# Optimization experiments

Measured on AMD Instinct MI355X. Metric: run time of the kernel, lower is better.

Reference implementation:

```python
import jax, jax.numpy as jnp
import numpy as np

N = 4096        # number of cells (graph nodes)
D = 128         # feature / embedding dim (isize)
NEIGHBOR = 15   # kNN column used for the distance cutoff
GAMMA = 8.0
OMEGA = 0.5


def setup_inputs() -> dict:
    key = jax.random.key(0)
    k = jax.random.split(key, 6)
    features = jax.random.normal(k[0], (N, D), dtype=jnp.float32)
    # sparse binary adjacency (~16 neighbors/node on average), stored dense
    adj = (jax.random.uniform(k[1], (N, N)) < 0.004).astype(jnp.float32)
    # symmetric positive pairwise distances
    d = jax.random.uniform(k[2], (N, N), minval=0.05, maxval=1.0)
    dis = ((d + d.T) * 0.5).astype(jnp.float32)
    scale = 1.0 / np.sqrt(D)
    W0 = (jax.random.normal(k[3], (D, D), dtype=jnp.float32) * scale)
    b0 = jnp.zeros((D,), jnp.float32)
    W1 = (jax.random.normal(k[4], (D, D), dtype=jnp.float32) * scale)
    b1 = jnp.zeros((D,), jnp.float32)
    return {"features": features, "adj": adj, "dis": dis,
            "W0": W0, "b0": b0, "W1": W1, "b1": b1}


def _gcn_layer(h, A, W, b):
    # torch_geometric GCNConv: sym-normalize (A + I), then X' = A_norm @ X @ W + b
    A_hat = A + jnp.eye(A.shape[0], dtype=A.dtype)
    deg = A_hat.sum(axis=1)
    dinv = jnp.where(deg > 0, 1.0 / jnp.sqrt(deg), 0.0)
    A_norm = dinv[:, None] * A_hat * dinv[None, :]
    return A_norm @ (h @ W) + b


def reference(features, adj, dis, W0, b0, W1, b1):
    eps = 1e-8
    # --- buffers precomputed in __init__ of the torch module ---
    d_sorted = jnp.sort(dis, axis=1)
    d_cut = jnp.median(d_sorted[:, NEIGHBOR])
    adj_mask = (dis > 0) & (dis <= d_cut)
    d_scaled = jnp.where(adj_mask, dis, jnp.inf) / d_cut
    s_d = jnp.exp(-GAMMA * d_scaled * d_scaled)   # 1/exp(g*d^2); exp(-inf)=0
    # --- internal_forward: 2 GCN layers on adj.T, relu between ---
    A = adj.T
    h = jax.nn.relu(_gcn_layer(features, A, W0, b0))
    h = _gcn_layer(h, A, W1, b1)
    # --- masked cosine similarity, blend with distance kernel ---
    h_norm = jnp.linalg.norm(h, axis=1, keepdims=True)   # [N,1]
    s1 = (h @ h.T) / (h_norm @ h_norm.T + eps)
    s1 = jnp.maximum(s1, 0.0)
    s = OMEGA * s1 + (1.0 - OMEGA) * s_d
    s = jnp.where(adj_mask, s, 0.0)
    # --- symmetric degree normalization D^{-1/2} S D^{-1/2} ---
    deg = s.sum(axis=1)
    dinv = jnp.where(deg > 0, 1.0 / jnp.sqrt(deg), 0.0)
    s_norm = dinv[:, None] * s * dinv[None, :]
    return s_norm, s
```

## Files before the change

kernel.cpp:

```cpp
#include <hip/hip_runtime.h>

#define N 4096
#define CAP 128

__global__ __launch_bounds__(256) void k_build(const float4* __restrict__ adj4,
                                               int* __restrict__ cnt1,
                                               int* __restrict__ nbr1) {
  int idx = blockIdx.x * blockDim.x + threadIdx.x;
  int stride = gridDim.x * blockDim.x;
  int total = N * N / 4;
  for (int k = idx; k < total; k += stride) {
    float4 a = adj4[k];
    int base = k << 2;
    int j  = base >> 12;
    int i0 = base & (N - 1);
    if (a.x != 0.f) { int p = atomicAdd(&cnt1[i0 + 0], 1); if (p < CAP) nbr1[(i0 + 0) * CAP + p] = j; }
    if (a.y != 0.f) { int p = atomicAdd(&cnt1[i0 + 1], 1); if (p < CAP) nbr1[(i0 + 1) * CAP + p] = j; }
    if (a.z != 0.f) { int p = atomicAdd(&cnt1[i0 + 2], 1); if (p < CAP) nbr1[(i0 + 2) * CAP + p] = j; }
    if (a.w != 0.f) { int p = atomicAdd(&cnt1[i0 + 3], 1); if (p < CAP) nbr1[(i0 + 3) * CAP + p] = j; }
  }
}

__global__ __launch_bounds__(256) void k_row16(const float* __restrict__ dis, float* __restrict__ r16) {
  __shared__ int lcnt;
  __shared__ float lval[CAP];
  int row = blockIdx.x, t = threadIdx.x;
  const float4* dp = (const float4*)(dis + (size_t)row * N);
  float T = 0.12f;
  int c = 0;
  for (int iter = 0; iter < 24; iter++) {
    if (t == 0) lcnt = 0;
    __syncthreads();
#pragma unroll
    for (int q = 0; q < 4; q++) {
      float4 d = dp[q * 256 + t];
      if (d.x <= T) { int p = atomicAdd(&lcnt, 1); if (p < CAP) lval[p] = d.x; }
      if (d.y <= T) { int p = atomicAdd(&lcnt, 1); if (p < CAP) lval[p] = d.y; }
      if (d.z <= T) { int p = atomicAdd(&lcnt, 1); if (p < CAP) lval[p] = d.z; }
      if (d.w <= T) { int p = atomicAdd(&lcnt, 1); if (p < CAP) lval[p] = d.w; }
    }
    __syncthreads();
    c = lcnt;
    __syncthreads();
    if (c >= 16 && c <= CAP) break;
    T = (c < 16) ? T * 2.0f : T * 0.5f;
  }
  if (t < c) {
    float v = lval[t];
    int less = 0;
    for (int j = 0; j < c; j++) {
      float u = lval[j];
      less += (u < v) || (u == v && j < t);
    }
    if (less == 15) r16[row] = v;
  }
}

__global__ __launch_bounds__(256) void k_median(const float* __restrict__ r16, float* __restrict__ scal) {
  __shared__ unsigned int keys[N];
  __shared__ int hist[256];
  __shared__ unsigned int s_prefix;
  __shared__ int s_rank;
  int t = threadIdx.x;
#pragma unroll
  for (int q = 0; q < 16; q++) keys[q * 256 + t] = __float_as_uint(r16[q * 256 + t]);
  __syncthreads();
  float res[2];
#pragma unroll
  for (int sel = 0; sel < 2; sel++) {
    if (t == 0) { s_rank = 2047 + sel; s_prefix = 0u; }
    __syncthreads();
    unsigned int mask = 0u;
    for (int shift = 24; shift >= 0; shift -= 8) {
      hist[t] = 0;
      __syncthreads();
      unsigned int prefix = s_prefix;
#pragma unroll
      for (int q = 0; q < 16; q++) {
        unsigned int k = keys[q * 256 + t];
        if ((k & mask) == prefix) atomicAdd(&hist[(k >> shift) & 255], 1);
      }
      __syncthreads();
      if (t == 0) {
        int r = s_rank, acc = 0, b = 0;
        for (; b < 256; b++) { if (acc + hist[b] > r) break; acc += hist[b]; }
        s_prefix = prefix | ((unsigned int)b << shift);
        s_rank = r - acc;
      }
      __syncthreads();
      mask |= (255u << shift);
    }
    res[sel] = __uint_as_float(s_prefix);
    __syncthreads();
  }
  if (t == 0) {
    float dcut = 0.5f * (res[0] + res[1]);
    scal[0] = dcut;
    scal[1] = 1.0f / dcut;
  }
}

__global__ __launch_bounds__(128) void k_gemm128(const float* __restrict__ X, const float* __restrict__ W,
                                                 const int* __restrict__ cnt1, float* __restrict__ out) {
  __shared__ float xs[8][128];
  int t = threadIdx.x;
  int r0 = blockIdx.x * 8;
#pragma unroll
  for (int r = 0; r < 8; r++) xs[r][t] = X[(size_t)(r0 + r) * 128 + t];
  __syncthreads();
  float acc[8] = {0.f, 0.f, 0.f, 0.f, 0.f, 0.f, 0.f, 0.f};
#pragma unroll 4
  for (int k = 0; k < 128; k++) {
    float wk = W[k * 128 + t];
#pragma unroll
    for (int r = 0; r < 8; r++) acc[r] = fmaf(xs[r][k], wk, acc[r]);
  }
#pragma unroll
  for (int r = 0; r < 8; r++) {
    float dv = 1.0f / sqrtf((float)cnt1[r0 + r] + 1.0f);
    out[(size_t)(r0 + r) * 128 + t] = dv * acc[r];
  }
}

__global__ __launch_bounds__(128) void k_spmm_relu(const float* __restrict__ Yd, const int* __restrict__ cnt,
                                                   const int* __restrict__ nbr,
                                                   const float* __restrict__ b, float* __restrict__ hout) {
  int row = blockIdx.x, t = threadIdx.x;
  int c = min(cnt[row], CAP);
  const int* lst = nbr + row * CAP;
  float acc = Yd[(size_t)row * 128 + t];
  for (int q = 0; q < c; q++) {
    int j = lst[q];
    acc += Yd[(size_t)j * 128 + t];
  }
  float dv = 1.0f / sqrtf((float)c + 1.0f);
  hout[(size_t)row * 128 + t] = fmaxf(dv * acc + b[t], 0.0f);
}

__global__ __launch_bounds__(128) void k_spmm_norm(const float* __restrict__ Yd, const int* __restrict__ cnt,
                                                   const int* __restrict__ nbr,
                                                   const float* __restrict__ b, float* __restrict__ hout,
                                                   float* __restrict__ hnorm) {
  __shared__ float red[2];
  int row = blockIdx.x, t = threadIdx.x;
  int c = min(cnt[row], CAP);
  const int* lst = nbr + row * CAP;
  float acc = Yd[(size_t)row * 128 + t];
  for (int q = 0; q < c; q++) {
    int j = lst[q];
    acc += Yd[(size_t)j * 128 + t];
  }
  float dv = 1.0f / sqrtf((float)c + 1.0f);
  float h = dv * acc + b[t];
  hout[(size_t)row * 128 + t] = h;
  float ss = h * h;
#pragma unroll
  for (int s = 32; s; s >>= 1) ss += __shfl_xor(ss, s, 64);
  if ((t & 63) == 0) red[t >> 6] = ss;
  __syncthreads();
  if (t == 0) hnorm[row] = sqrtf(red[0] + red[1]);
}

__global__ __launch_bounds__(256) void k_phaseA(const float* __restrict__ dis, const float* __restrict__ scal,
                                                float* __restrict__ s_out, int* __restrict__ cnt2,
                                                int* __restrict__ nbr2, float* __restrict__ sdsum) {
  __shared__ int lcnt;
  __shared__ int lidx[CAP];
  __shared__ float lred[4];
  int row = blockIdx.x, t = threadIdx.x;
  if (t == 0) lcnt = 0;
  __syncthreads();
  float dcut = scal[0];
  const float4* dp = (const float4*)(dis + (size_t)row * N);
  float4* sp = (float4*)(s_out + (size_t)row * N);
  float lsum = 0.f;
#pragma unroll
  for (int q = 0; q < 4; q++) {
    int k4 = q * 256 + t;
    float4 d = dp[k4];
    int jb = k4 << 2;
    float4 sv;
    float dd, s;
    dd = d.x; s = 0.f;
    if (dd > 0.f && dd <= dcut) { float r = dd / dcut; s = 0.5f * expf(-8.0f * r * r);
      int p = atomicAdd(&lcnt, 1); if (p < CAP) lidx[p] = jb + 0; lsum += s; }
    sv.x = s;
    dd = d.y; s = 0.f;
    if (dd > 0.f && dd <= dcut) { float r = dd / dcut; s = 0.5f * expf(-8.0f * r * r);
      int p = atomicAdd(&lcnt, 1); if (p < CAP) lidx[p] = jb + 1; lsum += s; }
    sv.y = s;
    dd = d.z; s = 0.f;
    if (dd > 0.f && dd <= dcut) { float r = dd / dcut; s = 0.5f * expf(-8.0f * r * r);
      int p = atomicAdd(&lcnt, 1); if (p < CAP) lidx[p] = jb + 2; lsum += s; }
    sv.z = s;
    dd = d.w; s = 0.f;
    if (dd > 0.f && dd <= dcut) { float r = dd / dcut; s = 0.5f * expf(-8.0f * r * r);
      int p = atomicAdd(&lcnt, 1); if (p < CAP) lidx[p] = jb + 3; lsum += s; }
    sv.w = s;
    sp[k4] = sv;
  }
#pragma unroll
  for (int s = 32; s; s >>= 1) lsum += __shfl_xor(lsum, s, 64);
  if ((t & 63) == 0) lred[t >> 6] = lsum;
  __syncthreads();
  int c = lcnt;
  if (t == 0) {
    sdsum[row] = lred[0] + lred[1] + lred[2] + lred[3];
    cnt2[row] = min(c, CAP);
  }
  for (int i = t; i < min(c, CAP); i += 256) nbr2[row * CAP + i] = lidx[i];
}

__global__ __launch_bounds__(256) void k_phaseB(const float* __restrict__ h, const float* __restrict__ hnorm,
                                                const int* __restrict__ cnt2, const int* __restrict__ nbr2,
                                                const float* __restrict__ sdsum, float* __restrict__ s_out,
                                                float* __restrict__ deg) {
  __shared__ float hi[128];
  __shared__ float wred[4];
  int row = blockIdx.x, t = threadIdx.x, wv = t >> 6, ln = t & 63;
  if (t < 128) hi[t] = h[(size_t)row * 128 + t];
  __syncthreads();
  int c = cnt2[row];
  float ni = hnorm[row];
  float wsum = 0.f;
  for (int idx = wv; idx < c; idx += 4) {
    int j = nbr2[row * CAP + idx];
    const float* hj = h + (size_t)j * 128;
    float p = hi[ln] * hj[ln] + hi[ln + 64] * hj[ln + 64];
#pragma unroll
    for (int s = 32; s; s >>= 1) p += __shfl_xor(p, s, 64);
    if (ln == 0) {
      float s1 = fmaxf(p / (ni * hnorm[j] + 1e-8f), 0.f);
      float v = 0.5f * s1;
      s_out[(size_t)row * N + j] += v;
      wsum += v;
    }
  }
  if (ln == 0) wred[wv] = wsum;
  __syncthreads();
  if (t == 0) deg[row] = sdsum[row] + wred[0] + wred[1] + wred[2] + wred[3];
}

__global__ __launch_bounds__(256) void k_norm(const float4* __restrict__ s4, const float* __restrict__ deg,
                                              float4* __restrict__ o4) {
  int idx = blockIdx.x * 256 + threadIdx.x;
  int i = idx >> 10;
  int jb = idx & 1023;
  float dgi = deg[i];
  float di = (dgi > 0.f) ? (1.0f / sqrtf(dgi)) : 0.f;
  float4 dg = ((const float4*)deg)[jb];
  float4 v = s4[idx];
  float4 r;
  r.x = di * ((dg.x > 0.f) ? (1.0f / sqrtf(dg.x)) : 0.f) * v.x;
  r.y = di * ((dg.y > 0.f) ? (1.0f / sqrtf(dg.y)) : 0.f) * v.y;
  r.z = di * ((dg.z > 0.f) ? (1.0f / sqrtf(dg.z)) : 0.f) * v.z;
  r.w = di * ((dg.w > 0.f) ? (1.0f / sqrtf(dg.w)) : 0.f) * v.w;
  o4[idx] = r;
}

extern "C" void kernel_launch(void* const* d_in, const int* in_sizes, int n_in,
                              void* d_out, int out_size, void* d_ws, size_t ws_size,
                              hipStream_t stream) {
  const float* features = (const float*)d_in[0];
  const float* adj      = (const float*)d_in[1];
  const float* dis      = (const float*)d_in[2];
  const float* b0       = (const float*)d_in[4];
  const float* W0       = (const float*)d_in[3];
  const float* W1       = (const float*)d_in[5];
  const float* b1       = (const float*)d_in[6];
  float* out    = (float*)d_out;
  float* s_half = out + (size_t)N * N;

  char* ws = (char*)d_ws;
  float* r16   = (float*)(ws + 0);
  int*   cnt1  = (int*)  (ws + 16384);
  float* sdsum = (float*)(ws + 49152);
  float* deg   = (float*)(ws + 65536);
  int*   cnt2  = (int*)  (ws + 98304);
  float* scal  = (float*)(ws + 114688);
  int*   nbr1  = (int*)  (ws + 131072);
  int*   nbr2  = (int*)  (ws + 131072 + 1 * 2097152);
  float* Yd0   = (float*)(ws + 131072 + 2 * 2097152);
  float* h1    = (float*)(ws + 131072 + 3 * 2097152);
  float* Y1d   = (float*)(ws + 131072 + 4 * 2097152);
  float* hbuf  = (float*)(ws + 131072 + 5 * 2097152);
  float* hnorm = (float*)(ws + 131072 + 6 * 2097152);

  hipMemsetAsync(cnt1, 0, N * sizeof(int), stream);

  k_build<<<2048, 256, 0, stream>>>((const float4*)adj, cnt1, nbr1);
  k_row16<<<N, 256, 0, stream>>>(dis, r16);
  k_median<<<1, 256, 0, stream>>>(r16, scal);
  k_gemm128<<<N / 8, 128, 0, stream>>>(features, W0, cnt1, Yd0);
  k_spmm_relu<<<N, 128, 0, stream>>>(Yd0, cnt1, nbr1, b0, h1);
  k_gemm128<<<N / 8, 128, 0, stream>>>(h1, W1, cnt1, Y1d);
  k_spmm_norm<<<N, 128, 0, stream>>>(Y1d, cnt1, nbr1, b1, hbuf, hnorm);
  k_phaseA<<<N, 256, 0, stream>>>(dis, scal, s_half, cnt2, nbr2, sdsum);
  k_phaseB<<<N, 256, 0, stream>>>(hbuf, hnorm, cnt2, nbr2, sdsum, s_half, deg);
  k_norm<<<(N * (N / 4)) / 256, 256, 0, stream>>>((const float4*)s_half, deg, (float4*)out);
}
```

Before: 398.7 us.

## Fuse stages, reuse kNN candidate lists, and write sparse similarity output directly

The ten kernels become six. The kNN threshold search, adjacency list build and first GEMM are merged into one heterogeneous launch. The row-16 search now saves its candidate distances and indices so the mask stage can usually skip re-reading the dense distance matrix. The dense intermediate S is no longer written, read back and renormalized: per-row sparse values and degrees are computed, and the final kernel zero-fills both outputs and scatters only the nonzeros. This removes several full N×N read/write passes. In exchange it relies on the 128-entry candidate cap and adds branchy multi-role blocks.

```diff
diff --git a/kernel.cpp b/kernel.cpp
--- a/kernel.cpp
+++ b/kernel.cpp
@@ -3,259 +3,296 @@
 #define N 4096
 #define CAP 128
 
-__global__ __launch_bounds__(256) void k_build(const float4* __restrict__ adj4,
-                                               int* __restrict__ cnt1,
-                                               int* __restrict__ nbr1) {
-  int idx = blockIdx.x * blockDim.x + threadIdx.x;
-  int stride = gridDim.x * blockDim.x;
-  int total = N * N / 4;
-  for (int k = idx; k < total; k += stride) {
-    float4 a = adj4[k];
-    int base = k << 2;
-    int j  = base >> 12;
-    int i0 = base & (N - 1);
-    if (a.x != 0.f) { int p = atomicAdd(&cnt1[i0 + 0], 1); if (p < CAP) nbr1[(i0 + 0) * CAP + p] = j; }
-    if (a.y != 0.f) { int p = atomicAdd(&cnt1[i0 + 1], 1); if (p < CAP) nbr1[(i0 + 1) * CAP + p] = j; }
-    if (a.z != 0.f) { int p = atomicAdd(&cnt1[i0 + 2], 1); if (p < CAP) nbr1[(i0 + 2) * CAP + p] = j; }
-    if (a.w != 0.f) { int p = atomicAdd(&cnt1[i0 + 3], 1); if (p < CAP) nbr1[(i0 + 3) * CAP + p] = j; }
-  }
-}
-
-__global__ __launch_bounds__(256) void k_row16(const float* __restrict__ dis, float* __restrict__ r16) {
-  __shared__ int lcnt;
-  __shared__ float lval[CAP];
-  int row = blockIdx.x, t = threadIdx.x;
-  const float4* dp = (const float4*)(dis + (size_t)row * N);
-  float T = 0.12f;
-  int c = 0;
-  for (int iter = 0; iter < 24; iter++) {
-    if (t == 0) lcnt = 0;
+__global__ __launch_bounds__(256) void K1(const float* __restrict__ dis,
+                                          const float4* __restrict__ adj4,
+                                          const float* __restrict__ X,
+                                          const float* __restrict__ W0,
+                                          int* __restrict__ cnt1, int* __restrict__ nbr1,
+                                          float* __restrict__ r16,
+                                          float* __restrict__ cand_d, int* __restrict__ cand_j,
+                                          int* __restrict__ cntc, float* __restrict__ Trow,
+                                          float* __restrict__ Y0) {
+  int b = blockIdx.x, t = threadIdx.x;
+  if (b < 4096) {
+    __shared__ int lcnt;
+    __shared__ float lval[CAP];
+    __shared__ int lidx[CAP];
+    int row = b;
+    const float4* dp = (const float4*)(dis + (size_t)row * N);
+    float T = 0.12f;
+    int c = 0;
+    for (int iter = 0; iter < 24; iter++) {
+      if (t == 0) lcnt = 0;
+      __syncthreads();
+#pragma unroll
+      for (int q = 0; q < 4; q++) {
+        float4 d = dp[q * 256 + t];
+        int jb = (q * 256 + t) << 2;
+        if (d.x <= T) { int p = atomicAdd(&lcnt, 1); if (p < CAP) { lval[p] = d.x; lidx[p] = jb + 0; } }
+        if (d.y <= T) { int p = atomicAdd(&lcnt, 1); if (p < CAP) { lval[p] = d.y; lidx[p] = jb + 1; } }
+        if (d.z <= T) { int p = atomicAdd(&lcnt, 1); if (p < CAP) { lval[p] = d.z; lidx[p] = jb + 2; } }
+        if (d.w <= T) { int p = atomicAdd(&lcnt, 1); if (p < CAP) { lval[p] = d.w; lidx[p] = jb + 3; } }
+      }
+      __syncthreads();
+      c = lcnt;
+      __syncthreads();
+      if (c >= 16 && c <= CAP) break;
+      T = (c < 16) ? T * 2.0f : T * 0.5f;
+    }
+    if (t < c) {
+      float v = lval[t];
+      int less = 0;
+      for (int j = 0; j < c; j++) {
+        float u = lval[j];
+        less += (u < v) || (u == v && j < t);
+      }
+      if (less == 15) r16[row] = v;
+    }
+    for (int k = t; k < c; k += 256) {
+      cand_d[row * CAP + k] = lval[k];
+      cand_j[row * CAP + k] = lidx[k];
+    }
+    if (t == 0) { cntc[row] = c; Trow[row] = T; }
+  } else if (b < 5120) {
+    int chunk = b - 4096;
+#pragma unroll
+    for (int q = 0; q < 16; q++) {
+      int k = chunk * 4096 + q * 256 + t;
+      float4 a = adj4[k];
+      int base = k << 2;
+      int j  = base >> 12;
+      int i0 = base & (N - 1);
+      if (a.x != 0.f) { int p = atomicAdd(&cnt1[i0 + 0], 1); if (p < CAP) nbr1[(i0 + 0) * CAP + p] = j; }
+      if (a.y != 0.f) { int p = atomicAdd(&cnt1[i0 + 1], 1); if (p < CAP) nbr1[(i0 + 1) * CAP + p] = j; }
+      if (a.z != 0.f) { int p = atomicAdd(&cnt1[i0 + 2], 1); if (p < CAP) nbr1[(i0 + 2) * CAP + p] = j; }
+      if (a.w != 0.f) { int p = atomicAdd(&cnt1[i0 + 3], 1); if (p < CAP) nbr1[(i0 + 3) * CAP + p] = j; }
+    }
+  } else {
+    __shared__ float xs[16][128];
+    int g = b - 5120;
+    int r0 = g * 16;
+    int col = t & 127, half = t >> 7;
+#pragma unroll
+    for (int q = 0; q < 8; q++) xs[q * 2 + half][col] = X[(size_t)(r0 + q * 2 + half) * 128 + col];
     __syncthreads();
-#pragma unroll
-    for (int q = 0; q < 4; q++) {
-      float4 d = dp[q * 256 + t];
-      if (d.x <= T) { int p = atomicAdd(&lcnt, 1); if (p < CAP) lval[p] = d.x; }
-      if (d.y <= T) { int p = atomicAdd(&lcnt, 1); if (p < CAP) lval[p] = d.y; }
-      if (d.z <= T) { int p = atomicAdd(&lcnt, 1); if (p < CAP) lval[p] = d.z; }
-      if (d.w <= T) { int p = atomicAdd(&lcnt, 1); if (p < CAP) lval[p] = d.w; }
-    }
+    float acc[8] = {0.f, 0.f, 0.f, 0.f, 0.f, 0.f, 0.f, 0.f};
+#pragma unroll 4
+    for (int k = 0; k < 128; k++) {
+      float wk = W0[k * 128 + col];
+#pragma unroll
+      for (int r = 0; r < 8; r++) acc[r] = fmaf(xs[half * 8 + r][k], wk, acc[r]);
+    }
+#pragma unroll
+    for (int r = 0; r < 8; r++) Y0[(size_t)(r0 + half * 8 + r) * 128 + col] = acc[r];
+  }
+}
+
+__global__ __launch_bounds__(256) void K2(const float* __restrict__ r16, float* __restrict__ scal,
+                                          const float* __restrict__ Y0, const int* __restrict__ cnt1,
+                                          const int* __restrict__ nbr1, const float* __restrict__ b0,
+                                          float* __restrict__ h1) {
+  int b = blockIdx.x, t = threadIdx.x;
+  if (b == 0) {
+    __shared__ unsigned int keys[N];
+    __shared__ int hist[256];
+    __shared__ unsigned int s_prefix;
+    __shared__ int s_rank;
+#pragma unroll
+    for (int q = 0; q < 16; q++) keys[q * 256 + t] = __float_as_uint(r16[q * 256 + t]);
     __syncthreads();
-    c = lcnt;
-    __syncthreads();
-    if (c >= 16 && c <= CAP) break;
-    T = (c < 16) ? T * 2.0f : T * 0.5f;
-  }
-  if (t < c) {
-    float v = lval[t];
-    int less = 0;
-    for (int j = 0; j < c; j++) {
-      float u = lval[j];
-      less += (u < v) || (u == v && j < t);
-    }
-    if (less == 15) r16[row] = v;
-  }
-}
-
-__global__ __launch_bounds__(256) void k_median(const float* __restrict__ r16, float* __restrict__ scal) {
-  __shared__ unsigned int keys[N];
-  __shared__ int hist[256];
-  __shared__ unsigned int s_prefix;
-  __shared__ int s_rank;
+    float res[2];
+#pragma unroll
+    for (int sel = 0; sel < 2; sel++) {
+      if (t == 0) { s_rank = 2047 + sel; s_prefix = 0u; }
+      __syncthreads();
+      unsigned int mask = 0u;
+      for (int shift = 24; shift >= 0; shift -= 8) {
+        hist[t] = 0;
+        __syncthreads();
+        unsigned int prefix = s_prefix;
+#pragma unroll
+        for (int q = 0; q < 16; q++) {
+          unsigned int k = keys[q * 256 + t];
+          if ((k & mask) == prefix) atomicAdd(&hist[(k >> shift) & 255], 1);
+        }
+        __syncthreads();
+        if (t == 0) {
+          int r = s_rank, acc = 0, bb = 0;
+          for (; bb < 256; bb++) { if (acc + hist[bb] > r) break; acc += hist[bb]; }
+          s_prefix = prefix | ((unsigned int)bb << shift);
+          s_rank = r - acc;
+        }
+        __syncthreads();
+        mask |= (255u << shift);
+      }
+      res[sel] = __uint_as_float(s_prefix);
+      __syncthreads();
+    }
+    if (t == 0) {
+      float dcut = 0.5f * (res[0] + res[1]);
+      scal[0] = dcut;
+      scal[1] = 1.0f / dcut;
+    }
+  } else {
+    int row = 2 * (b - 1) + (t >> 7);
+    int col = t & 127;
+    int ci = min(cnt1[row], CAP);
+    float dvi = 1.0f / sqrtf((float)ci + 1.0f);
+    const int* lst = nbr1 + row * CAP;
+    float acc = dvi * Y0[(size_t)row * 128 + col];
+    for (int q = 0; q < ci; q++) {
+      int j = lst[q];
+      float dvj = 1.0f / sqrtf((float)min(cnt1[j], CAP) + 1.0f);
+      acc += dvj * Y0[(size_t)j * 128 + col];
+    }
+    h1[(size_t)row * 128 + col] = fmaxf(dvi * acc + b0[col], 0.0f);
+  }
+}
+
+__global__ __launch_bounds__(256) void K3(const float* __restrict__ X, const float* __restrict__ W1,
+                                          float* __restrict__ Y1) {
+  __shared__ float xs[16][128];
   int t = threadIdx.x;
-#pragma unroll
-  for (int q = 0; q < 16; q++) keys[q * 256 + t] = __float_as_uint(r16[q * 256 + t]);
-  __syncthreads();
-  float res[2];
-#pragma unroll
-  for (int sel = 0; sel < 2; sel++) {
-    if (t == 0) { s_rank = 2047 + sel; s_prefix = 0u; }
-    __syncthreads();
-    unsigned int mask = 0u;
-    for (int shift = 24; shift >= 0; shift -= 8) {
-      hist[t] = 0;
-      __syncthreads();
-      unsigned int prefix = s_prefix;
-#pragma unroll
-      for (int q = 0; q < 16; q++) {
-        unsigned int k = keys[q * 256 + t];
-        if ((k & mask) == prefix) atomicAdd(&hist[(k >> shift) & 255], 1);
-      }
-      __syncthreads();
-      if (t == 0) {
-        int r = s_rank, acc = 0, b = 0;
-        for (; b < 256; b++) { if (acc + hist[b] > r) break; acc += hist[b]; }
-        s_prefix = prefix | ((unsigned int)b << shift);
-        s_rank = r - acc;
-      }
-      __syncthreads();
-      mask |= (255u << shift);
-    }
-    res[sel] = __uint_as_float(s_prefix);
-    __syncthreads();
-  }
-  if (t == 0) {
-    float dcut = 0.5f * (res[0] + res[1]);
-    scal[0] = dcut;
-    scal[1] = 1.0f / dcut;
-  }
-}
-
-__global__ __launch_bounds__(128) void k_gemm128(const float* __restrict__ X, const float* __restrict__ W,
-                                                 const int* __restrict__ cnt1, float* __restrict__ out) {
-  __shared__ float xs[8][128];
-  int t = threadIdx.x;
-  int r0 = blockIdx.x * 8;
-#pragma unroll
-  for (int r = 0; r < 8; r++) xs[r][t] = X[(size_t)(r0 + r) * 128 + t];
+  int r0 = blockIdx.x * 16;
+  int col = t & 127, half = t >> 7;
+#pragma unroll
+  for (int q = 0; q < 8; q++) xs[q * 2 + half][col] = X[(size_t)(r0 + q * 2 + half) * 128 + col];
   __syncthreads();
   float acc[8] = {0.f, 0.f, 0.f, 0.f, 0.f, 0.f, 0.f, 0.f};
 #pragma unroll 4
   for (int k = 0; k < 128; k++) {
-    float wk = W[k * 128 + t];
-#pragma unroll
-    for (int r = 0; r < 8; r++) acc[r] = fmaf(xs[r][k], wk, acc[r]);
-  }
-#pragma unroll
-  for (int r = 0; r < 8; r++) {
-    float dv = 1.0f / sqrtf((float)cnt1[r0 + r] + 1.0f);
-    out[(size_t)(r0 + r) * 128 + t] = dv * acc[r];
-  }
-}
-
-__global__ __launch_bounds__(128) void k_spmm_relu(const float* __restrict__ Yd, const int* __restrict__ cnt,
-                                                   const int* __restrict__ nbr,
-                                                   const float* __restrict__ b, float* __restrict__ hout) {
-  int row = blockIdx.x, t = threadIdx.x;
-  int c = min(cnt[row], CAP);
-  const int* lst = nbr + row * CAP;
-  float acc = Yd[(size_t)row * 128 + t];
-  for (int q = 0; q < c; q++) {
+    float wk = W1[k * 128 + col];
+#pragma unroll
+    for (int r = 0; r < 8; r++) acc[r] = fmaf(xs[half * 8 + r][k], wk, acc[r]);
+  }
+#pragma unroll
+  for (int r = 0; r < 8; r++) Y1[(size_t)(r0 + half * 8 + r) * 128 + col] = acc[r];
+}
+
+__global__ __launch_bounds__(256) void K4(const float* __restrict__ Y1, const int* __restrict__ cnt1,
+                                          const int* __restrict__ nbr1, const float* __restrict__ b1,
+                                          float* __restrict__ hbuf, float* __restrict__ hnorm) {
+  __shared__ float red[4];
+  int b = blockIdx.x, t = threadIdx.x;
+  int row = 2 * b + (t >> 7);
+  int col = t & 127;
+  int ci = min(cnt1[row], CAP);
+  float dvi = 1.0f / sqrtf((float)ci + 1.0f);
+  const int* lst = nbr1 + row * CAP;
+  float acc = dvi * Y1[(size_t)row * 128 + col];
+  for (int q = 0; q < ci; q++) {
     int j = lst[q];
-    acc += Yd[(size_t)j * 128 + t];
-  }
-  float dv = 1.0f / sqrtf((float)c + 1.0f);
-  hout[(size_t)row * 128 + t] = fmaxf(dv * acc + b[t], 0.0f);
-}
-
-__global__ __launch_bounds__(128) void k_spmm_norm(const float* __restrict__ Yd, const int* __restrict__ cnt,
-                                                   const int* __restrict__ nbr,
-                                                   const float* __restrict__ b, float* __restrict__ hout,
-                                                   float* __restrict__ hnorm) {
-  __shared__ float red[2];
-  int row = blockIdx.x, t = threadIdx.x;
-  int c = min(cnt[row], CAP);
-  const int* lst = nbr + row * CAP;
-  float acc = Yd[(size_t)row * 128 + t];
-  for (int q = 0; q < c; q++) {
-    int j = lst[q];
-    acc += Yd[(size_t)j * 128 + t];
-  }
-  float dv = 1.0f / sqrtf((float)c + 1.0f);
-  float h = dv * acc + b[t];
-  hout[(size_t)row * 128 + t] = h;
+    float dvj = 1.0f / sqrtf((float)min(cnt1[j], CAP) + 1.0f);
+    acc += dvj * Y1[(size_t)j * 128 + col];
+  }
+  float h = dvi * acc + b1[col];
+  hbuf[(size_t)row * 128 + col] = h;
   float ss = h * h;
 #pragma unroll
   for (int s = 32; s; s >>= 1) ss += __shfl_xor(ss, s, 64);
   if ((t & 63) == 0) red[t >> 6] = ss;
   __syncthreads();
-  if (t == 0) hnorm[row] = sqrtf(red[0] + red[1]);
-}
-
-__global__ __launch_bounds__(256) void k_phaseA(const float* __restrict__ dis, const float* __restrict__ scal,
-                                                float* __restrict__ s_out, int* __restrict__ cnt2,
-                                                int* __restrict__ nbr2, float* __restrict__ sdsum) {
-  __shared__ int lcnt;
-  __shared__ int lidx[CAP];
-  __shared__ float lred[4];
-  int row = blockIdx.x, t = threadIdx.x;
-  if (t == 0) lcnt = 0;
-  __syncthreads();
-  float dcut = scal[0];
-  const float4* dp = (const float4*)(dis + (size_t)row * N);
-  float4* sp = (float4*)(s_out + (size_t)row * N);
-  float lsum = 0.f;
-#pragma unroll
-  for (int q = 0; q < 4; q++) {
-    int k4 = q * 256 + t;
-    float4 d = dp[k4];
-    int jb = k4 << 2;
-    float4 sv;
-    float dd, s;
-    dd = d.x; s = 0.f;
-    if (dd > 0.f && dd <= dcut) { float r = dd / dcut; s = 0.5f * expf(-8.0f * r * r);
-      int p = atomicAdd(&lcnt, 1); if (p < CAP) lidx[p] = jb + 0; lsum += s; }
-    sv.x = s;
-    dd = d.y; s = 0.f;
-    if (dd > 0.f && dd <= dcut) { float r = dd / dcut; s = 0.5f * expf(-8.0f * r * r);
-      int p = atomicAdd(&lcnt, 1); if (p < CAP) lidx[p] = jb + 1; lsum += s; }
-    sv.y = s;
-    dd = d.z; s = 0.f;
-    if (dd > 0.f && dd <= dcut) { float r = dd / dcut; s = 0.5f * expf(-8.0f * r * r);
-      int p = atomicAdd(&lcnt, 1); if (p < CAP) lidx[p] = jb + 2; lsum += s; }
-    sv.z = s;
-    dd = d.w; s = 0.f;
-    if (dd > 0.f && dd <= dcut) { float r = dd / dcut; s = 0.5f * expf(-8.0f * r * r);
-      int p = atomicAdd(&lcnt, 1); if (p < CAP) lidx[p] = jb + 3; lsum += s; }
-    sv.w = s;
-    sp[k4] = sv;
-  }
-#pragma unroll
-  for (int s = 32; s; s >>= 1) lsum += __shfl_xor(lsum, s, 64);
-  if ((t & 63) == 0) lred[t >> 6] = lsum;
-  __syncthreads();
-  int c = lcnt;
-  if (t == 0) {
-    sdsum[row] = lred[0] + lred[1] + lred[2] + lred[3];
-    cnt2[row] = min(c, CAP);
-  }
-  for (int i = t; i < min(c, CAP); i += 256) nbr2[row * CAP + i] = lidx[i];
-}
-
-__global__ __launch_bounds__(256) void k_phaseB(const float* __restrict__ h, const float* __restrict__ hnorm,
-                                                const int* __restrict__ cnt2, const int* __restrict__ nbr2,
-                                                const float* __restrict__ sdsum, float* __restrict__ s_out,
-                                                float* __restrict__ deg) {
+  if (t == 0)   hnorm[row]     = sqrtf(red[0] + red[1]);
+  if (t == 128) hnorm[row]     = sqrtf(red[2] + red[3]);
+}
+
+__global__ __launch_bounds__(256) void K5(const float* __restrict__ dis, const float* __restrict__ scal,
+                                          const float* __restrict__ cand_d, const int* __restrict__ cand_j,
+                                          const int* __restrict__ cntc, const float* __restrict__ Trow,
+                                          const float* __restrict__ hbuf, const float* __restrict__ hnorm,
+                                          float* __restrict__ vals, int* __restrict__ jdx,
+                                          int* __restrict__ cnt2, float* __restrict__ deg) {
+  __shared__ float cd[CAP];
+  __shared__ int cj[CAP];
+  __shared__ float sdv[CAP];
+  __shared__ int sj[CAP];
+  __shared__ int ccnt, scnt;
   __shared__ float hi[128];
   __shared__ float wred[4];
-  int row = blockIdx.x, t = threadIdx.x, wv = t >> 6, ln = t & 63;
-  if (t < 128) hi[t] = h[(size_t)row * 128 + t];
-  __syncthreads();
-  int c = cnt2[row];
+  int row = blockIdx.x, t = threadIdx.x;
+  int wv = t >> 6, ln = t & 63;
+  float dcut = scal[0];
+  if (t == 0) { scnt = 0; ccnt = 0; }
+  if (t < 128) hi[t] = hbuf[(size_t)row * 128 + t];
+  __syncthreads();
+  int c1;
+  if (Trow[row] >= dcut) {
+    c1 = cntc[row];
+    for (int k = t; k < c1; k += 256) { cd[k] = cand_d[row * CAP + k]; cj[k] = cand_j[row * CAP + k]; }
+  } else {
+    const float4* dp = (const float4*)(dis + (size_t)row * N);
+#pragma unroll
+    for (int q = 0; q < 4; q++) {
+      float4 d = dp[q * 256 + t];
+      int jb = (q * 256 + t) << 2;
+      if (d.x <= dcut) { int p = atomicAdd(&ccnt, 1); if (p < CAP) { cd[p] = d.x; cj[p] = jb + 0; } }
+      if (d.y <= dcut) { int p = atomicAdd(&ccnt, 1); if (p < CAP) { cd[p] = d.y; cj[p] = jb + 1; } }
+      if (d.z <= dcut) { int p = atomicAdd(&ccnt, 1); if (p < CAP) { cd[p] = d.z; cj[p] = jb + 2; } }
+      if (d.w <= dcut) { int p = atomicAdd(&ccnt, 1); if (p < CAP) { cd[p] = d.w; cj[p] = jb + 3; } }
+    }
+    __syncthreads();
+    c1 = min(ccnt, CAP);
+  }
+  __syncthreads();
+  if (t < c1) {
+    float d = cd[t];
+    if (d > 0.f && d <= dcut) {
+      float r = d / dcut;
+      int p = atomicAdd(&scnt, 1);
+      sdv[p] = 0.5f * expf(-8.0f * r * r);
+      sj[p] = cj[t];
+    }
+  }
+  __syncthreads();
+  int c2 = scnt;
   float ni = hnorm[row];
   float wsum = 0.f;
-  for (int idx = wv; idx < c; idx += 4) {
-    int j = nbr2[row * CAP + idx];
-    const float* hj = h + (size_t)j * 128;
+  for (int idx = wv; idx < c2; idx += 4) {
+    int j = sj[idx];
+    const float* hj = hbuf + (size_t)j * 128;
     float p = hi[ln] * hj[ln] + hi[ln + 64] * hj[ln + 64];
 #pragma unroll
     for (int s = 32; s; s >>= 1) p += __shfl_xor(p, s, 64);
     if (ln == 0) {
       float s1 = fmaxf(p / (ni * hnorm[j] + 1e-8f), 0.f);
-      float v = 0.5f * s1;
-      s_out[(size_t)row * N + j] += v;
+      float v = sdv[idx] + 0.5f * s1;
+      vals[row * CAP + idx] = v;
+      jdx[row * CAP + idx] = j;
       wsum += v;
     }
   }
   if (ln == 0) wred[wv] = wsum;
   __syncthreads();
-  if (t == 0) deg[row] = sdsum[row] + wred[0] + wred[1] + wred[2] + wred[3];
-}
-
-__global__ __launch_bounds__(256) void k_norm(const float4* __restrict__ s4, const float* __restrict__ deg,
-                                              float4* __restrict__ o4) {
-  int idx = blockIdx.x * 256 + threadIdx.x;
-  int i = idx >> 10;
-  int jb = idx & 1023;
-  float dgi = deg[i];
+  if (t == 0) {
+    deg[row] = wred[0] + wred[1] + wred[2] + wred[3];
+    cnt2[row] = c2;
+  }
+}
+
+__global__ __launch_bounds__(256) void K6(const float* __restrict__ vals, const int* __restrict__ jdx,
+                                          const int* __restrict__ cnt2, const float* __restrict__ deg,
+                                          float* __restrict__ s_norm_out, float* __restrict__ s_out) {
+  int row = blockIdx.x, t = threadIdx.x;
+  float dgi = deg[row];
   float di = (dgi > 0.f) ? (1.0f / sqrtf(dgi)) : 0.f;
-  float4 dg = ((const float4*)deg)[jb];
-  float4 v = s4[idx];
-  float4 r;
-  r.x = di * ((dg.x > 0.f) ? (1.0f / sqrtf(dg.x)) : 0.f) * v.x;
-  r.y = di * ((dg.y > 0.f) ? (1.0f / sqrtf(dg.y)) : 0.f) * v.y;
-  r.z = di * ((dg.z > 0.f) ? (1.0f / sqrtf(dg.z)) : 0.f) * v.z;
-  r.w = di * ((dg.w > 0.f) ? (1.0f / sqrtf(dg.w)) : 0.f) * v.w;
-  o4[idx] = r;
+  float4 z = {0.f, 0.f, 0.f, 0.f};
+  float4* sp = (float4*)(s_out + (size_t)row * N);
+  float4* op = (float4*)(s_norm_out + (size_t)row * N);
+#pragma unroll
+  for (int q = 0; q < 4; q++) {
+    sp[q * 256 + t] = z;
+    op[q * 256 + t] = z;
+  }
+  __syncthreads();
+  int c2 = cnt2[row];
+  if (t < c2) {
+    int j = jdx[row * CAP + t];
+    float v = vals[row * CAP + t];
+    s_out[(size_t)row * N + j] = v;
+    float dgj = deg[j];
+    float dj = (dgj > 0.f) ? (1.0f / sqrtf(dgj)) : 0.f;
+    s_norm_out[(size_t)row * N + j] = di * dj * v;
+  }
 }
 
 extern "C" void kernel_launch(void* const* d_in, const int* in_sizes, int n_in,
@@ -264,8 +301,8 @@
   const float* features = (const float*)d_in[0];
   const float* adj      = (const float*)d_in[1];
   const float* dis      = (const float*)d_in[2];
+  const float* W0       = (const float*)d_in[3];
   const float* b0       = (const float*)d_in[4];
-  const float* W0       = (const float*)d_in[3];
   const float* W1       = (const float*)d_in[5];
   const float* b1       = (const float*)d_in[6];
   float* out    = (float*)d_out;
@@ -274,28 +311,30 @@
   char* ws = (char*)d_ws;
   float* r16   = (float*)(ws + 0);
   int*   cnt1  = (int*)  (ws + 16384);
-  float* sdsum = (float*)(ws + 49152);
+  int*   cntc  = (int*)  (ws + 32768);
+  float* Trow  = (float*)(ws + 49152);
   float* deg   = (float*)(ws + 65536);
-  int*   cnt2  = (int*)  (ws + 98304);
-  float* scal  = (float*)(ws + 114688);
-  int*   nbr1  = (int*)  (ws + 131072);
-  int*   nbr2  = (int*)  (ws + 131072 + 1 * 2097152);
-  float* Yd0   = (float*)(ws + 131072 + 2 * 2097152);
-  float* h1    = (float*)(ws + 131072 + 3 * 2097152);
-  float* Y1d   = (float*)(ws + 131072 + 4 * 2097152);
-  float* hbuf  = (float*)(ws + 131072 + 5 * 2097152);
-  float* hnorm = (float*)(ws + 131072 + 6 * 2097152);
+  int*   cnt2  = (int*)  (ws + 81920);
+  float* scal  = (float*)(ws + 98304);
+  float* hnorm = (float*)(ws + 114688);
+  int*   nbr1  = (int*)  (ws + 131072 + 0 * 2097152);
+  float* cand_dv=(float*)(ws + 131072 + 1 * 2097152);
+  int*   cand_j= (int*)  (ws + 131072 + 2 * 2097152);
+  float* vals  = (float*)(ws + 131072 + 3 * 2097152);
+  int*   jdx   = (int*)  (ws + 131072 + 4 * 2097152);
+  float* Y0    = (float*)(ws + 131072 + 5 * 2097152);
+  float* h1    = (float*)(ws + 131072 + 6 * 2097152);
+  float* Y1    = (float*)(ws + 131072 + 7 * 2097152);
+  float* hbuf  = (float*)(ws + 131072 + 8 * 2097152);
 
   hipMemsetAsync(cnt1, 0, N * sizeof(int), stream);
 
-  k_build<<<2048, 256, 0, stream>>>((const float4*)adj, cnt1, nbr1);
-  k_row16<<<N, 256, 0, stream>>>(dis, r16);
-  k_median<<<1, 256, 0, stream>>>(r16, scal);
-  k_gemm128<<<N / 8, 128, 0, stream>>>(features, W0, cnt1, Yd0);
-  k_spmm_relu<<<N, 128, 0, stream>>>(Yd0, cnt1, nbr1, b0, h1);
-  k_gemm128<<<N / 8, 128, 0, stream>>>(h1, W1, cnt1, Y1d);
-  k_spmm_norm<<<N, 128, 0, stream>>>(Y1d, cnt1, nbr1, b1, hbuf, hnorm);
-  k_phaseA<<<N, 256, 0, stream>>>(dis, scal, s_half, cnt2, nbr2, sdsum);
-  k_phaseB<<<N, 256, 0, stream>>>(hbuf, hnorm, cnt2, nbr2, sdsum, s_half, deg);
-  k_norm<<<(N * (N / 4)) / 256, 256, 0, stream>>>((const float4*)s_half, deg, (float4*)out);
-}
+  K1<<<5376, 256, 0, stream>>>(dis, (const float4*)adj, features, W0,
+                               cnt1, nbr1, r16, cand_dv, cand_j, cntc, Trow, Y0);
+  K2<<<2049, 256, 0, stream>>>(r16, scal, Y0, cnt1, nbr1, b0, h1);
+  K3<<<256, 256, 0, stream>>>(h1, W1, Y1);
+  K4<<<2048, 256, 0, stream>>>(Y1, cnt1, nbr1, b1, hbuf, hnorm);
+  K5<<<4096, 256, 0, stream>>>(dis, scal, cand_dv, cand_j, cntc, Trow,
+                               hbuf, hnorm, vals, jdx, cnt2, deg);
+  K6<<<4096, 256, 0, stream>>>(vals, jdx, cnt2, deg, out, s_half);
+}
```

New measurement: 375.6 us. -5.8%, faster.
